# Optimization experiments

Hardware: AMD Instinct MI355X
Metric: run time of the kernel (lower is better)

## Reference

```python
import jax, jax.numpy as jnp
import numpy as np

GRID_SIZE = 300


def setup_inputs() -> dict:
    key = jax.random.key(0)
    k1, k2 = jax.random.split(key)
    N, input_dim, out_dim = 2048, 256, 256
    x = jax.random.normal(k1, (N, input_dim), dtype=jnp.float32)
    scale = 1.0 / (np.sqrt(input_dim) * np.sqrt(GRID_SIZE))
    coeffs = jax.random.normal(k2, (2, out_dim, input_dim, GRID_SIZE), dtype=jnp.float32) * scale
    bias = jnp.zeros((1, out_dim), dtype=jnp.float32)
    return {"x": x, "coeffs": coeffs, "bias": bias}


def reference(x, coeffs, bias):
    # x: [N, I]; coeffs: [2, J, I, K]; bias: [1, J]
    grid_size = coeffs.shape[-1]
    k = jnp.arange(1, grid_size + 1, dtype=x.dtype)            # [K]
    ang = x[:, :, None] * k                                    # [N, I, K]
    c = jnp.cos(ang)
    s = jnp.sin(ang)
    # einsum('dbik,djik->bj') with d=2 split into cos/sin parts
    y = jnp.einsum('bik,jik->bj', c, coeffs[0]) + jnp.einsum('bik,jik->bj', s, coeffs[1])
    y = y + bias
    return y
```

## Files before the change

### kernel.cpp

```cpp
#include <hip/hip_runtime.h>
#include <stdint.h>

#define NB 2048
#define NI 256
#define NJ 256
#define GK 300
#define KPAD 320
#define KK_PER_I (2*KPAD)
#define NKC (NI*KK_PER_I/32)
#define SPLITK 32
#define II_PER_S (NI / SPLITK)
#define BM 128
#define BN 256

typedef __bf16 bf16x8 __attribute__((ext_vector_type(8)));
typedef __bf16 bf16x2 __attribute__((ext_vector_type(2)));
typedef float  f32x4  __attribute__((ext_vector_type(4)));
typedef __attribute__((address_space(1))) const unsigned int gu32;
typedef __attribute__((address_space(3))) unsigned int lu32;

__device__ __forceinline__ void sincos2pi(float ang, float& c, float& s) {
  float r = ang * 0.15915494309189535f;
  r = r - floorf(r);
  c = __builtin_amdgcn_cosf(r);
  s = __builtin_amdgcn_sinf(r);
}

__global__ __launch_bounds__(256) void convert_b(const float* __restrict__ coeffs,
                                                 unsigned int* __restrict__ bw) {
  const int bid = blockIdx.x;
  const int i  = bid >> 4;
  const int jt = bid & 15;
  const int t  = (int)threadIdx.x;
  const int n  = t & 15;
  const int gl = t >> 4;
  const int j  = jt * 16 + n;

  const float4* r0 = (const float4*)(coeffs + (size_t)(j * NI + i) * GK);
  const float4* r1 = (const float4*)(coeffs + (size_t)((NJ + j) * NI + i) * GK);

  #pragma unroll
  for (int p = 0; p < 5; p++) {
    const int g = p * 16 + gl;
    uint4 w = {0u, 0u, 0u, 0u};
    if (g < GK / 4) {
      float4 a = r0[g];
      float4 b = r1[g];
      bf16x2 p0; p0.x = (__bf16)a.x; p0.y = (__bf16)b.x;
      bf16x2 p1; p1.x = (__bf16)a.y; p1.y = (__bf16)b.y;
      bf16x2 p2; p2.x = (__bf16)a.z; p2.y = (__bf16)b.z;
      bf16x2 p3; p3.x = (__bf16)a.w; p3.y = (__bf16)b.w;
      w.x = __builtin_bit_cast(unsigned int, p0);
      w.y = __builtin_bit_cast(unsigned int, p1);
      w.z = __builtin_bit_cast(unsigned int, p2);
      w.w = __builtin_bit_cast(unsigned int, p3);
    }
    const int kc = i * 20 + (g >> 2);
    const unsigned int idx = ((unsigned int)(kc * 16 + jt) << 8) + ((g & 3) << 6) + (n << 2);
    *(uint4*)(bw + idx) = w;
  }
}

__global__ __launch_bounds__(256) void init_out(const float* __restrict__ bias,
                                                float* __restrict__ out) {
  const int tid = blockIdx.x * 256 + threadIdx.x;
  float4 b = ((const float4*)bias)[tid & 63];
  ((float4*)out)[tid] = b;
}

__global__ __launch_bounds__(256, 2) void fkan_gemm(const float* __restrict__ x,
                                                    const unsigned int* __restrict__ bw,
                                                    float* __restrict__ out) {
  __shared__ uint4 lds4[3072];
  char* lds = (char*)lds4;

  const int bid = blockIdx.x;
  const int mt = bid & 15;
  const int s  = bid >> 4;
  const int m0 = mt * BM;

  const int t    = (int)threadIdx.x;
  const int lane = t & 63;
  const int wave = t >> 6;

  const int gn  = t & 15;
  const int gmt = (t >> 4) & 7;
  const int gkc = t >> 7;
  const int grow = gmt * 16 + gn;
  const float* xptr = x + (m0 + grow) * NI;
  const unsigned int abase = (unsigned int)((gkc * 8 + gmt) * 1024 + gn * 16);

  const int wr = wave >> 1;
  const int wc = wave & 1;

  f32x4 acc[4][8];
  #pragma unroll
  for (int mm = 0; mm < 4; mm++)
    #pragma unroll
    for (int nn = 0; nn < 8; nn++)
      acc[mm][nn] = (f32x4){0.f, 0.f, 0.f, 0.f};

  const int kc0 = s * (NKC / SPLITK);

  #pragma unroll 1
  for (int ii = 0; ii < II_PER_S; ii++) {
    const int i = s * II_PER_S + ii;
    const float xv = xptr[i];
    float c1, s1, c32, s32, ccur, scur;
    sincos2pi(xv, c1, s1);
    sincos2pi(32.f * xv, c32, s32);
    sincos2pi(xv * (float)(gkc * 16 + 1), ccur, scur);

    #pragma unroll 1
    for (int t10 = 0; t10 < 10; t10++) {
      __syncthreads();

      float cc = ccur, ss = scur;
      #pragma unroll
      for (int q = 0; q < 4; q++) {
        uint4 w;
        #pragma unroll
        for (int p = 0; p < 4; p++) {
          bf16x2 pk; pk.x = (__bf16)cc; pk.y = (__bf16)ss;
          ((unsigned int*)&w)[p] = __builtin_bit_cast(unsigned int, pk);
          float nc = cc * c1 - ss * s1;
          ss = ss * c1 + cc * s1;
          cc = nc;
        }
        *(uint4*)(lds + abase + q * 256) = w;
      }
      {
        float nc = ccur * c32 - scur * s32;
        scur = scur * c32 + ccur * s32;
        ccur = nc;
      }

      const int kc = kc0 + ii * (KK_PER_I / 32) + t10 * 2;
      #pragma unroll
      for (int q2 = 0; q2 < 8; q2++) {
        const int idx = wave * 8 + q2;
        const int kcoff = idx >> 4;
        const int jtoff = idx & 15;
        const unsigned int* src = bw + ((((kc + kcoff) * 16) + jtoff) << 8)
                                     + lane * 4;
        unsigned int* dst = (unsigned int*)(lds + 16384 + idx * 1024);
        __builtin_amdgcn_global_load_lds((gu32*)src, (lu32*)dst, 16, 0, 0);
      }

      __syncthreads();

      #pragma unroll
      for (int ks = 0; ks < 2; ks++) {
        bf16x8 af[4];
        #pragma unroll
        for (int mm = 0; mm < 4; mm++)
          af[mm] = *(bf16x8*)(lds + (ks * 8 + wr * 4 + mm) * 1024 + lane * 16);
        #pragma unroll
        for (int nn = 0; nn < 8; nn++) {
          bf16x8 bfr = *(bf16x8*)(lds + 16384 + (ks * 16 + wc * 8 + nn) * 1024 + lane * 16);
          #pragma unroll
          for (int mm = 0; mm < 4; mm++)
            acc[mm][nn] = __builtin_amdgcn_mfma_f32_16x16x32_bf16(
                af[mm], bfr, acc[mm][nn], 0, 0, 0);
        }
      }
    }
  }

  const int r0 = m0 + wr * 64 + ((lane >> 4) << 2);
  const int c0 = wc * 128 + (lane & 15);
  #pragma unroll
  for (int mm = 0; mm < 4; mm++)
    #pragma unroll
    for (int nn = 0; nn < 8; nn++)
      #pragma unroll
      for (int r = 0; r < 4; r++)
        atomicAdd(&out[(r0 + mm * 16 + r) * NJ + c0 + nn * 16], acc[mm][nn][r]);
}

extern "C" void kernel_launch(void* const* d_in, const int* in_sizes, int n_in,
                              void* d_out, int out_size, void* d_ws, size_t ws_size,
                              hipStream_t stream) {
  const float* x      = (const float*)d_in[0];
  const float* coeffs = (const float*)d_in[1];
  const float* bias   = (const float*)d_in[2];
  float* out = (float*)d_out;
  unsigned int* bw = (unsigned int*)d_ws;

  convert_b<<<dim3(NI * 16), dim3(256), 0, stream>>>(coeffs, bw);
  init_out<<<dim3(NB * NJ / 4 / 256), dim3(256), 0, stream>>>(bias, out);
  fkan_gemm<<<dim3(16 * SPLITK), dim3(256), 0, stream>>>(x, bw, out);
}
```

Baseline: 451.1 us.

## Drop LDS staging; generate A fragments in registers and prefetch B directly

The GEMM kernel no longer stages the sin/cos A tile or the bf16 B tile through shared memory. Each lane computes its own A fragment values in registers with angle-rotation recurrences, and loads its B fragments straight from global memory with a one-chunk register prefetch (double buffer). This removes both __syncthreads barriers and all LDS traffic per chunk. In exchange, each wave duplicates the trig work, B reads go uncoalesced through L2 with no sharing across waves, and register pressure rises, which could hurt occupancy.

```diff
diff --git a/kernel.cpp b/kernel.cpp
--- a/kernel.cpp
+++ b/kernel.cpp
@@ -8,22 +8,31 @@
 #define KPAD 320
 #define KK_PER_I (2*KPAD)
 #define NKC (NI*KK_PER_I/32)
+#define CH_PER_I 20
 #define SPLITK 32
 #define II_PER_S (NI / SPLITK)
 #define BM 128
-#define BN 256
 
 typedef __bf16 bf16x8 __attribute__((ext_vector_type(8)));
 typedef __bf16 bf16x2 __attribute__((ext_vector_type(2)));
 typedef float  f32x4  __attribute__((ext_vector_type(4)));
-typedef __attribute__((address_space(1))) const unsigned int gu32;
-typedef __attribute__((address_space(3))) unsigned int lu32;
 
 __device__ __forceinline__ void sincos2pi(float ang, float& c, float& s) {
   float r = ang * 0.15915494309189535f;
   r = r - floorf(r);
   c = __builtin_amdgcn_cosf(r);
   s = __builtin_amdgcn_sinf(r);
+}
+
+__device__ __forceinline__ unsigned int pkbf(float c, float s) {
+  bf16x2 p; p.x = (__bf16)c; p.y = (__bf16)s;
+  return __builtin_bit_cast(unsigned int, p);
+}
+
+__device__ __forceinline__ void rot(float& c, float& s, float cr, float sr) {
+  float nc = c * cr - s * sr;
+  s = s * cr + c * sr;
+  c = nc;
 }
 
 __global__ __launch_bounds__(256) void convert_b(const float* __restrict__ coeffs,
@@ -46,14 +55,10 @@
     if (g < GK / 4) {
       float4 a = r0[g];
       float4 b = r1[g];
-      bf16x2 p0; p0.x = (__bf16)a.x; p0.y = (__bf16)b.x;
-      bf16x2 p1; p1.x = (__bf16)a.y; p1.y = (__bf16)b.y;
-      bf16x2 p2; p2.x = (__bf16)a.z; p2.y = (__bf16)b.z;
-      bf16x2 p3; p3.x = (__bf16)a.w; p3.y = (__bf16)b.w;
-      w.x = __builtin_bit_cast(unsigned int, p0);
-      w.y = __builtin_bit_cast(unsigned int, p1);
-      w.z = __builtin_bit_cast(unsigned int, p2);
-      w.w = __builtin_bit_cast(unsigned int, p3);
+      w.x = pkbf(a.x, b.x);
+      w.y = pkbf(a.y, b.y);
+      w.z = pkbf(a.z, b.z);
+      w.w = pkbf(a.w, b.w);
     }
     const int kc = i * 20 + (g >> 2);
     const unsigned int idx = ((unsigned int)(kc * 16 + jt) << 8) + ((g & 3) << 6) + (n << 2);
@@ -69,11 +74,8 @@
 }
 
 __global__ __launch_bounds__(256, 2) void fkan_gemm(const float* __restrict__ x,
-                                                    const unsigned int* __restrict__ bw,
+                                                    const uint4* __restrict__ bw4,
                                                     float* __restrict__ out) {
-  __shared__ uint4 lds4[3072];
-  char* lds = (char*)lds4;
-
   const int bid = blockIdx.x;
   const int mt = bid & 15;
   const int s  = bid >> 4;
@@ -82,16 +84,10 @@
   const int t    = (int)threadIdx.x;
   const int lane = t & 63;
   const int wave = t >> 6;
-
-  const int gn  = t & 15;
-  const int gmt = (t >> 4) & 7;
-  const int gkc = t >> 7;
-  const int grow = gmt * 16 + gn;
-  const float* xptr = x + (m0 + grow) * NI;
-  const unsigned int abase = (unsigned int)((gkc * 8 + gmt) * 1024 + gn * 16);
-
   const int wr = wave >> 1;
   const int wc = wave & 1;
+  const int q  = lane >> 4;
+  const int ln = lane & 15;
 
   f32x4 acc[4][8];
   #pragma unroll
@@ -100,75 +96,63 @@
     for (int nn = 0; nn < 8; nn++)
       acc[mm][nn] = (f32x4){0.f, 0.f, 0.f, 0.f};
 
-  const int kc0 = s * (NKC / SPLITK);
+  const uint4* bptr = bw4 + (size_t)(wc * 8) * 64 + lane;
+
+  int kc = s * (NKC / SPLITK);
+  uint4 bcur[8], bnxt[8];
+  #pragma unroll
+  for (int nn = 0; nn < 8; nn++) bcur[nn] = bptr[(size_t)kc * 1024 + nn * 64];
+
+  float stc[4], sts[4], c1a[4], s1a[4], cDa[4], sDa[4];
 
   #pragma unroll 1
   for (int ii = 0; ii < II_PER_S; ii++) {
     const int i = s * II_PER_S + ii;
-    const float xv = xptr[i];
-    float c1, s1, c32, s32, ccur, scur;
-    sincos2pi(xv, c1, s1);
-    sincos2pi(32.f * xv, c32, s32);
-    sincos2pi(xv * (float)(gkc * 16 + 1), ccur, scur);
+    #pragma unroll
+    for (int mm = 0; mm < 4; mm++) {
+      const float xv = x[(m0 + wr * 64 + mm * 16 + ln) * NI + i];
+      sincos2pi(xv, c1a[mm], s1a[mm]);
+      sincos2pi(13.f * xv, cDa[mm], sDa[mm]);
+      sincos2pi(xv * (float)(q * 4 + 1), stc[mm], sts[mm]);
+    }
 
-    #pragma unroll 1
-    for (int t10 = 0; t10 < 10; t10++) {
-      __syncthreads();
+    #pragma unroll 2
+    for (int c = 0; c < CH_PER_I; c++) {
+      const int kcn = (kc + 1 < NKC) ? kc + 1 : kc;
+      #pragma unroll
+      for (int nn = 0; nn < 8; nn++)
+        bnxt[nn] = bptr[(size_t)kcn * 1024 + nn * 64];
 
-      float cc = ccur, ss = scur;
+      bf16x8 af[4];
       #pragma unroll
-      for (int q = 0; q < 4; q++) {
-        uint4 w;
-        #pragma unroll
-        for (int p = 0; p < 4; p++) {
-          bf16x2 pk; pk.x = (__bf16)cc; pk.y = (__bf16)ss;
-          ((unsigned int*)&w)[p] = __builtin_bit_cast(unsigned int, pk);
-          float nc = cc * c1 - ss * s1;
-          ss = ss * c1 + cc * s1;
-          cc = nc;
-        }
-        *(uint4*)(lds + abase + q * 256) = w;
-      }
-      {
-        float nc = ccur * c32 - scur * s32;
-        scur = scur * c32 + ccur * s32;
-        ccur = nc;
+      for (int mm = 0; mm < 4; mm++) {
+        float cc = stc[mm], ss = sts[mm];
+        uint4 u;
+        u.x = pkbf(cc, ss);
+        rot(cc, ss, c1a[mm], s1a[mm]); u.y = pkbf(cc, ss);
+        rot(cc, ss, c1a[mm], s1a[mm]); u.z = pkbf(cc, ss);
+        rot(cc, ss, c1a[mm], s1a[mm]); u.w = pkbf(cc, ss);
+        rot(cc, ss, cDa[mm], sDa[mm]); stc[mm] = cc; sts[mm] = ss;
+        af[mm] = __builtin_bit_cast(bf16x8, u);
       }
 
-      const int kc = kc0 + ii * (KK_PER_I / 32) + t10 * 2;
       #pragma unroll
-      for (int q2 = 0; q2 < 8; q2++) {
-        const int idx = wave * 8 + q2;
-        const int kcoff = idx >> 4;
-        const int jtoff = idx & 15;
-        const unsigned int* src = bw + ((((kc + kcoff) * 16) + jtoff) << 8)
-                                     + lane * 4;
-        unsigned int* dst = (unsigned int*)(lds + 16384 + idx * 1024);
-        __builtin_amdgcn_global_load_lds((gu32*)src, (lu32*)dst, 16, 0, 0);
+      for (int nn = 0; nn < 8; nn++) {
+        const bf16x8 bfr = __builtin_bit_cast(bf16x8, bcur[nn]);
+        #pragma unroll
+        for (int mm = 0; mm < 4; mm++)
+          acc[mm][nn] = __builtin_amdgcn_mfma_f32_16x16x32_bf16(
+              af[mm], bfr, acc[mm][nn], 0, 0, 0);
       }
 
-      __syncthreads();
-
       #pragma unroll
-      for (int ks = 0; ks < 2; ks++) {
-        bf16x8 af[4];
-        #pragma unroll
-        for (int mm = 0; mm < 4; mm++)
-          af[mm] = *(bf16x8*)(lds + (ks * 8 + wr * 4 + mm) * 1024 + lane * 16);
-        #pragma unroll
-        for (int nn = 0; nn < 8; nn++) {
-          bf16x8 bfr = *(bf16x8*)(lds + 16384 + (ks * 16 + wc * 8 + nn) * 1024 + lane * 16);
-          #pragma unroll
-          for (int mm = 0; mm < 4; mm++)
-            acc[mm][nn] = __builtin_amdgcn_mfma_f32_16x16x32_bf16(
-                af[mm], bfr, acc[mm][nn], 0, 0, 0);
-        }
-      }
+      for (int nn = 0; nn < 8; nn++) bcur[nn] = bnxt[nn];
+      kc++;
     }
   }
 
-  const int r0 = m0 + wr * 64 + ((lane >> 4) << 2);
-  const int c0 = wc * 128 + (lane & 15);
+  const int r0 = m0 + wr * 64 + q * 4;
+  const int c0 = wc * 128 + ln;
   #pragma unroll
   for (int mm = 0; mm < 4; mm++)
     #pragma unroll
@@ -189,5 +173,5 @@
 
   convert_b<<<dim3(NI * 16), dim3(256), 0, stream>>>(coeffs, bw);
   init_out<<<dim3(NB * NJ / 4 / 256), dim3(256), 0, stream>>>(bias, out);
-  fkan_gemm<<<dim3(16 * SPLITK), dim3(256), 0, stream>>>(x, bw, out);
+  fkan_gemm<<<dim3(16 * SPLITK), dim3(256), 0, stream>>>(x, (const uint4*)bw, out);
 }
```

After: 435.4 us. 3.5% less time.
